# Performance work log

Hardware: AMD Instinct MI355X
Metric: run time of the kernel (lower is better)

Reference implementation:

```python
import jax, jax.numpy as jnp
import numpy as np

N_NODES = 50000
N_EDGES = 800000
IN_DIM = 128
OUT_DIM = 128
N_HEADS = 4
HEAD_DIM = OUT_DIM // N_HEADS
EDGE_EMBED_DIM = 16
LN_EPS = 1e-5


def setup_inputs() -> dict:
    key = jax.random.key(0)
    ks = jax.random.split(key, 10)
    x = jax.random.normal(ks[0], (N_NODES, IN_DIM), dtype=jnp.float32)
    edge_index = jax.random.randint(ks[1], (2, N_EDGES), 0, N_NODES, dtype=jnp.int32)
    edge_type = jax.random.randint(ks[2], (N_EDGES,), 0, 3, dtype=jnp.int32)
    # parameters (xavier-ish scaling)
    W = jax.random.normal(ks[3], (OUT_DIM, IN_DIM), dtype=jnp.float32) * (1.0 / np.sqrt(IN_DIM))
    a_src = jax.random.normal(ks[4], (N_HEADS, HEAD_DIM), dtype=jnp.float32) * (1.0 / np.sqrt(HEAD_DIM))
    a_dst = jax.random.normal(ks[5], (N_HEADS, HEAD_DIM), dtype=jnp.float32) * (1.0 / np.sqrt(HEAD_DIM))
    a_edge = jax.random.normal(ks[6], (N_HEADS, EDGE_EMBED_DIM), dtype=jnp.float32) * (1.0 / np.sqrt(EDGE_EMBED_DIM))
    edge_embed = jax.random.normal(ks[7], (3, EDGE_EMBED_DIM), dtype=jnp.float32)
    ln_gamma = jnp.ones((OUT_DIM,), dtype=jnp.float32)
    ln_beta = jnp.zeros((OUT_DIM,), dtype=jnp.float32)
    return {"x": x, "edge_index": edge_index, "edge_type": edge_type,
            "W": W, "a_src": a_src, "a_dst": a_dst, "a_edge": a_edge,
            "edge_embed": edge_embed, "ln_gamma": ln_gamma, "ln_beta": ln_beta}


def reference(x, edge_index, edge_type, W, a_src, a_dst, a_edge, edge_embed, ln_gamma, ln_beta):
    N = x.shape[0]
    h = x @ W.T                                   # [N, out_dim]
    hh = h.reshape(N, N_HEADS, HEAD_DIM)          # [N, H, D]
    src, dst = edge_index[0], edge_index[1]       # [E]

    # per-node attention projections, then gather (avoids gathering full [E,H,D] twice)
    alpha_src = jnp.einsum('nhd,hd->nh', hh, a_src)   # [N, H]
    alpha_dst = jnp.einsum('nhd,hd->nh', hh, a_dst)   # [N, H]
    e_score = edge_embed[edge_type] @ a_edge.T        # [E, H]

    attn = alpha_src[src] + alpha_dst[dst] + e_score  # [E, H]
    attn = jax.nn.leaky_relu(attn, negative_slope=0.2)

    # segment softmax over incoming edges of each dst node
    attn_max = jax.ops.segment_max(attn, dst, num_segments=N)    # [N, H]
    attn_max = jnp.maximum(attn_max, -1e9)                       # match torch init fill
    attn_exp = jnp.exp(attn - attn_max[dst])                     # [E, H]
    attn_sum = jax.ops.segment_sum(attn_exp, dst, num_segments=N)
    attn_norm = attn_exp / (attn_sum[dst] + 1e-10)               # [E, H]

    # weighted scatter-aggregation (dropout is identity in eval)
    weighted = hh[src] * attn_norm[:, :, None]                   # [E, H, D]
    out = jax.ops.segment_sum(weighted, dst, num_segments=N)     # [N, H, D]
    out = out.reshape(N, OUT_DIM) + h                            # residual

    # LayerNorm over last dim
    mu = jnp.mean(out, axis=-1, keepdims=True)
    var = jnp.var(out, axis=-1, keepdims=True)
    out = (out - mu) * jax.lax.rsqrt(var + LN_EPS)
    return out * ln_gamma + ln_beta
```

## Files before the change

kernel.cpp:

```cpp
#include <hip/hip_runtime.h>

#define N_NODES 50000
#define N_EDGES 800000
#define IN_DIM 128
#define OUT_DIM 128
#define N_HEADS 4
#define HEAD_DIM 32
#define LN_EPS 1e-5f

#define WS_HB    0
#define WS_ASRC  3200000
#define WS_ADST  3400000
#define WS_ETAB  3600000
#define WS_DEG   3600016
#define WS_AVTAB 3650016
#define WS_OFFS  3650528
#define WS_PARTS 3700528
#define WS_EPACK 3700592
#define WS_RANK  4500608

#define SCAN_BLOCKS 49

typedef __bf16 bf16x8 __attribute__((ext_vector_type(8)));
typedef float  f32x4  __attribute__((ext_vector_type(4)));

__device__ __forceinline__ unsigned short f2bf(float f) {
    unsigned int u = __float_as_uint(f);
    u += 0x7FFF + ((u >> 16) & 1);
    return (unsigned short)(u >> 16);
}
#define BFLO(u) __uint_as_float((unsigned int)(u) << 16)
#define BFHI(u) __uint_as_float((unsigned int)(u) & 0xFFFF0000u)
#define LRELU(c) ((c) > 0.f ? (c) : 0.2f * (c))

__global__ __launch_bounds__(256) void count_prep_kernel(
    const int* __restrict__ dsts, int* __restrict__ deg, int* __restrict__ rank,
    const float* __restrict__ W, const float* __restrict__ a_src,
    const float* __restrict__ a_dst, const float* __restrict__ edge_embed,
    const float* __restrict__ a_edge, float* __restrict__ etab,
    unsigned short* __restrict__ avtab)
{
    int gid = blockIdx.x * 256 + threadIdx.x;
    if (gid < 12) {
        int t = gid >> 2, hh = gid & 3;
        float s = 0.f;
        for (int k = 0; k < 16; ++k) s += edge_embed[t * 16 + k] * a_edge[hh * 16 + k];
        etab[t * 4 + hh] = s;
    }
    if (gid < 1024) {
        int c8 = gid & 7, k = gid >> 3;
        int hh = c8 & 3;
        const float* av = (c8 < 4) ? a_src : a_dst;
        float s = 0.f;
        #pragma unroll 8
        for (int dd = 0; dd < 32; ++dd)
            s += W[(hh * 32 + dd) * 128 + k] * av[hh * 32 + dd];
        int kblk = k >> 5, g = (k & 31) >> 3, j = k & 7;
        avtab[((kblk * 64) + g * 16 + c8) * 8 + j] = f2bf(s);
    }
    if (gid < N_EDGES) rank[gid] = atomicAdd(&deg[dsts[gid]], 1);
}

__global__ __launch_bounds__(256) void gemm_mfma_kernel(
    const float* __restrict__ x, const float* __restrict__ W,
    const unsigned short* __restrict__ avtab,
    unsigned short* __restrict__ hb,
    float* __restrict__ alpha_src, float* __restrict__ alpha_dst)
{
    __shared__ bf16x8 wlds[2048];
    int tid = threadIdx.x;
    for (int f = tid; f < 2048; f += 256) {
        int ct = f >> 8, kb = (f >> 6) & 3, ln = f & 63;
        int d = ct * 16 + (ln & 15);
        int kbase = kb * 32 + ((ln >> 4) << 3);
        const float* wp = W + d * 128 + kbase;
        float4 w0 = *(const float4*)wp;
        float4 w1 = *(const float4*)(wp + 4);
        bf16x8 v;
        v[0] = (__bf16)w0.x; v[1] = (__bf16)w0.y; v[2] = (__bf16)w0.z; v[3] = (__bf16)w0.w;
        v[4] = (__bf16)w1.x; v[5] = (__bf16)w1.y; v[6] = (__bf16)w1.z; v[7] = (__bf16)w1.w;
        wlds[f] = v;
    }
    int lane = tid & 63, wid = tid >> 6;
    bf16x8 avf[4];
    const bf16x8* avp = (const bf16x8*)avtab;
    #pragma unroll
    for (int kb = 0; kb < 4; ++kb) avf[kb] = avp[kb * 64 + lane];
    __syncthreads();

    int r = lane & 15, g = lane >> 4;
    int tile = blockIdx.x * 4 + wid;
    if (tile >= N_NODES / 16) return;
    {
        const float* xp = x + ((size_t)tile * 16 + r) * 128 + g * 8;
        bf16x8 af[4];
        #pragma unroll
        for (int kb = 0; kb < 4; ++kb) {
            float4 x0 = *(const float4*)(xp + kb * 32);
            float4 x1 = *(const float4*)(xp + kb * 32 + 4);
            bf16x8 v;
            v[0] = (__bf16)x0.x; v[1] = (__bf16)x0.y; v[2] = (__bf16)x0.z; v[3] = (__bf16)x0.w;
            v[4] = (__bf16)x1.x; v[5] = (__bf16)x1.y; v[6] = (__bf16)x1.z; v[7] = (__bf16)x1.w;
            af[kb] = v;
        }
        f32x4 aacc = {0.f, 0.f, 0.f, 0.f};
        #pragma unroll
        for (int kb = 0; kb < 4; ++kb)
            aacc = __builtin_amdgcn_mfma_f32_16x16x32_bf16(af[kb], avf[kb], aacc, 0, 0, 0);

        int orow = tile * 16 + g * 4;
        #pragma unroll
        for (int ct = 0; ct < 8; ++ct) {
            f32x4 acc = {0.f, 0.f, 0.f, 0.f};
            #pragma unroll
            for (int kb = 0; kb < 4; ++kb)
                acc = __builtin_amdgcn_mfma_f32_16x16x32_bf16(af[kb], wlds[(ct * 4 + kb) * 64 + lane], acc, 0, 0, 0);
            #pragma unroll
            for (int q = 0; q < 4; ++q)
                hb[(size_t)(orow + q) * 128 + ct * 16 + r] = f2bf(acc[q]);
        }
        if (r < 8) {
            float* ap = (r < 4) ? (alpha_src + (r & 3)) : (alpha_dst + (r & 3));
            #pragma unroll
            for (int q = 0; q < 4; ++q)
                ap[(size_t)(orow + q) * 4] = aacc[q];
        }
    }
}

__global__ __launch_bounds__(1024) void scan_part_kernel(
    const int* __restrict__ deg, int* __restrict__ offs, int* __restrict__ parts)
{
    __shared__ int wsum[16];
    int i = blockIdx.x * 1024 + threadIdx.x;
    int lane = threadIdx.x & 63;
    int wid  = threadIdx.x >> 6;
    int v = (i < N_NODES) ? deg[i] : 0;
    int xinc = v;
    #pragma unroll
    for (int d = 1; d < 64; d <<= 1) {
        int y = __shfl_up(xinc, d);
        if (lane >= d) xinc += y;
    }
    if (lane == 63) wsum[wid] = xinc;
    __syncthreads();
    if (wid == 0) {
        int sv = (lane < 16) ? wsum[lane] : 0;
        #pragma unroll
        for (int d = 1; d < 16; d <<= 1) {
            int y = __shfl_up(sv, d);
            if (lane >= d) sv += y;
        }
        if (lane < 16) wsum[lane] = sv;
    }
    __syncthreads();
    int woff = (wid > 0) ? wsum[wid - 1] : 0;
    if (i < N_NODES) offs[i] = woff + xinc - v;
    if (threadIdx.x == 0) parts[blockIdx.x] = wsum[15];
}

__global__ __launch_bounds__(1024) void scan_add_kernel(
    int* __restrict__ offs, const int* __restrict__ parts)
{
    __shared__ int pre_s;
    if (threadIdx.x < 64) {
        int v = ((int)threadIdx.x < (int)blockIdx.x) ? parts[threadIdx.x] : 0;
        #pragma unroll
        for (int off = 32; off >= 1; off >>= 1) v += __shfl_xor(v, off);
        if (threadIdx.x == 0) pre_s = v;
    }
    __syncthreads();
    int i = blockIdx.x * 1024 + threadIdx.x;
    if (i < N_NODES) offs[i] += pre_s;
}

__global__ void fill_kernel(const int* __restrict__ srcs, const int* __restrict__ dsts,
                            const int* __restrict__ etype, const int* __restrict__ rank,
                            const int* __restrict__ offs, unsigned int* __restrict__ epack)
{
    int e = blockIdx.x * 256 + threadIdx.x;
    if (e < N_EDGES) {
        int d = dsts[e];
        int p = offs[d] + rank[e];
        epack[p] = (unsigned int)srcs[e] | ((unsigned int)etype[e] << 16);
    }
}

__global__ __launch_bounds__(256) void aggregate_kernel(
    const unsigned short* __restrict__ hb, const float* __restrict__ alpha_src,
    const float* __restrict__ alpha_dst, const float* __restrict__ etab,
    const unsigned int* __restrict__ epack, const int* __restrict__ offs,
    const float* __restrict__ gamma, const float* __restrict__ beta,
    float* __restrict__ out)
{
    int lane = threadIdx.x & 63;
    int wid  = threadIdx.x >> 6;
    int half = lane >> 5;
    int l5   = lane & 31;
    int n = blockIdx.x * 8 + wid * 2 + half;
    if (n >= N_NODES) return;

    int e0 = offs[n];
    int e1 = (n == N_NODES - 1) ? N_EDGES : offs[n + 1];
    int deg = e1 - e0;

    int g  = l5 >> 3;
    int sl = l5 & 7;
    int headL = sl >> 1;

    float ad_h = alpha_dst[(size_t)n * 4 + headL];
    float et0 = etab[0 * 4 + headL];
    float et1 = etab[1 * 4 + headL];
    float et2 = etab[2 * 4 + headL];

    float s = 0.f;
    float acc[16];
    #pragma unroll
    for (int k = 0; k < 16; ++k) acc[k] = 0.f;

    const unsigned int* ep = epack + e0;
    for (int j = g; j < deg; j += 4) {
        unsigned int p = ep[j];
        int si = p & 0xFFFF;
        int t  = p >> 16;
        float asv = alpha_src[(size_t)si * 4 + headL];
        const uint4* hp = (const uint4*)(hb + ((size_t)si << 7) + (sl << 4));
        uint4 hA = hp[0];
        uint4 hB = hp[1];
        float ev = (t == 0) ? et0 : ((t == 1) ? et1 : et2);
        float c = LRELU(asv + ad_h + ev);
        float w = __expf(c);
        s += w;
        acc[0]  += w * BFLO(hA.x); acc[1]  += w * BFHI(hA.x);
        acc[2]  += w * BFLO(hA.y); acc[3]  += w * BFHI(hA.y);
        acc[4]  += w * BFLO(hA.z); acc[5]  += w * BFHI(hA.z);
        acc[6]  += w * BFLO(hA.w); acc[7]  += w * BFHI(hA.w);
        acc[8]  += w * BFLO(hB.x); acc[9]  += w * BFHI(hB.x);
        acc[10] += w * BFLO(hB.y); acc[11] += w * BFHI(hB.y);
        acc[12] += w * BFLO(hB.z); acc[13] += w * BFHI(hB.z);
        acc[14] += w * BFLO(hB.w); acc[15] += w * BFHI(hB.w);
    }

    #pragma unroll
    for (int k = 0; k < 16; ++k) {
        acc[k] += __shfl_xor(acc[k], 8);
        acc[k] += __shfl_xor(acc[k], 16);
    }
    s += __shfl_xor(s, 8);
    s += __shfl_xor(s, 16);
    float rs = 1.0f / (s + 1e-10f);

    const uint4* rp = (const uint4*)(hb + ((size_t)n << 7) + (sl << 4));
    uint4 r0 = rp[0];
    uint4 r1 = rp[1];
    float o[16];
    o[0]  = acc[0]  * rs + BFLO(r0.x); o[1]  = acc[1]  * rs + BFHI(r0.x);
    o[2]  = acc[2]  * rs + BFLO(r0.y); o[3]  = acc[3]  * rs + BFHI(r0.y);
    o[4]  = acc[4]  * rs + BFLO(r0.z); o[5]  = acc[5]  * rs + BFHI(r0.z);
    o[6]  = acc[6]  * rs + BFLO(r0.w); o[7]  = acc[7]  * rs + BFHI(r0.w);
    o[8]  = acc[8]  * rs + BFLO(r1.x); o[9]  = acc[9]  * rs + BFHI(r1.x);
    o[10] = acc[10] * rs + BFLO(r1.y); o[11] = acc[11] * rs + BFHI(r1.y);
    o[12] = acc[12] * rs + BFLO(r1.z); o[13] = acc[13] * rs + BFHI(r1.z);
    o[14] = acc[14] * rs + BFLO(r1.w); o[15] = acc[15] * rs + BFHI(r1.w);

    float lsum = 0.f;
    #pragma unroll
    for (int k = 0; k < 16; ++k) lsum += o[k];
    #pragma unroll
    for (int off = 4; off >= 1; off >>= 1) lsum += __shfl_xor(lsum, off);
    float mean = lsum * (1.0f / 128.0f);
    float vs = 0.f;
    #pragma unroll
    for (int k = 0; k < 16; ++k) { float d = o[k] - mean; vs += d * d; }
    #pragma unroll
    for (int off = 4; off >= 1; off >>= 1) vs += __shfl_xor(vs, off);
    float inv = rsqrtf(vs * (1.0f / 128.0f) + LN_EPS);

    float4 gv = *(const float4*)(gamma + sl * 16 + g * 4);
    float4 bv = *(const float4*)(beta  + sl * 16 + g * 4);
    float4 wv;
    wv.x = (o[g * 4 + 0] - mean) * inv * gv.x + bv.x;
    wv.y = (o[g * 4 + 1] - mean) * inv * gv.y + bv.y;
    wv.z = (o[g * 4 + 2] - mean) * inv * gv.z + bv.z;
    wv.w = (o[g * 4 + 3] - mean) * inv * gv.w + bv.w;
    *(float4*)(out + (size_t)n * OUT_DIM + sl * 16 + g * 4) = wv;
}

extern "C" void kernel_launch(void* const* d_in, const int* in_sizes, int n_in,
                              void* d_out, int out_size, void* d_ws, size_t ws_size,
                              hipStream_t stream)
{
    const float* x          = (const float*)d_in[0];
    const int*   edge_index = (const int*)d_in[1];
    const int*   etype      = (const int*)d_in[2];
    const float* W          = (const float*)d_in[3];
    const float* a_src      = (const float*)d_in[4];
    const float* a_dst      = (const float*)d_in[5];
    const float* a_edge     = (const float*)d_in[6];
    const float* edge_embed = (const float*)d_in[7];
    const float* gamma      = (const float*)d_in[8];
    const float* beta       = (const float*)d_in[9];

    float* ws = (float*)d_ws;
    unsigned short* hb = (unsigned short*)(ws + WS_HB);
    float* asrc = ws + WS_ASRC;
    float* adst = ws + WS_ADST;
    float* etab = ws + WS_ETAB;
    int*   deg  = (int*)d_ws + WS_DEG;
    unsigned short* avtab = (unsigned short*)((int*)d_ws + WS_AVTAB);
    int*   offs = (int*)d_ws + WS_OFFS;
    int*   parts= (int*)d_ws + WS_PARTS;
    unsigned int* epack = (unsigned int*)d_ws + WS_EPACK;
    int*   rank = (int*)d_ws + WS_RANK;

    const int* srcs = edge_index;
    const int* dsts = edge_index + N_EDGES;

    hipMemsetAsync(deg, 0, N_NODES * sizeof(int) + 2048 * sizeof(unsigned short), stream);

    count_prep_kernel<<<(N_EDGES + 255) / 256, 256, 0, stream>>>(
        dsts, deg, rank, W, a_src, a_dst, edge_embed, a_edge, etab, avtab);
    gemm_mfma_kernel<<<(N_NODES / 16 + 3) / 4, 256, 0, stream>>>(x, W, avtab, hb, asrc, adst);
    scan_part_kernel<<<SCAN_BLOCKS, 1024, 0, stream>>>(deg, offs, parts);
    scan_add_kernel<<<SCAN_BLOCKS, 1024, 0, stream>>>(offs, parts);
    fill_kernel<<<(N_EDGES + 255) / 256, 256, 0, stream>>>(srcs, dsts, etype, rank, offs, epack);
    aggregate_kernel<<<(N_NODES + 7) / 8, 256, 0, stream>>>(
        hb, asrc, adst, etab, epack, offs, gamma, beta, (float*)d_out);
}
```

Measured before the change: 118.7 us.

## Merge degree counting into GEMM launch and replace memset with prep kernel zeroing

```diff
diff --git a/kernel.cpp b/kernel.cpp
--- a/kernel.cpp
+++ b/kernel.cpp
@@ -20,6 +20,8 @@
 #define WS_RANK  4500608
 
 #define SCAN_BLOCKS 49
+#define GEMM_BLOCKS 512
+#define COUNT_BLOCKS 3125
 
 typedef __bf16 bf16x8 __attribute__((ext_vector_type(8)));
 typedef float  f32x4  __attribute__((ext_vector_type(4)));
@@ -33,14 +35,15 @@
 #define BFHI(u) __uint_as_float((unsigned int)(u) & 0xFFFF0000u)
 #define LRELU(c) ((c) > 0.f ? (c) : 0.2f * (c))
 
-__global__ __launch_bounds__(256) void count_prep_kernel(
-    const int* __restrict__ dsts, int* __restrict__ deg, int* __restrict__ rank,
+__global__ __launch_bounds__(256) void prep_zero_kernel(
+    int4* __restrict__ degv,
     const float* __restrict__ W, const float* __restrict__ a_src,
     const float* __restrict__ a_dst, const float* __restrict__ edge_embed,
     const float* __restrict__ a_edge, float* __restrict__ etab,
     unsigned short* __restrict__ avtab)
 {
     int gid = blockIdx.x * 256 + threadIdx.x;
+    if (gid < N_NODES / 4) degv[gid] = make_int4(0, 0, 0, 0);
     if (gid < 12) {
         int t = gid >> 2, hh = gid & 3;
         float s = 0.f;
@@ -58,17 +61,24 @@
         int kblk = k >> 5, g = (k & 31) >> 3, j = k & 7;
         avtab[((kblk * 64) + g * 16 + c8) * 8 + j] = f2bf(s);
     }
-    if (gid < N_EDGES) rank[gid] = atomicAdd(&deg[dsts[gid]], 1);
-}
-
-__global__ __launch_bounds__(256) void gemm_mfma_kernel(
+}
+
+__global__ __launch_bounds__(256) void gemm_count_kernel(
     const float* __restrict__ x, const float* __restrict__ W,
     const unsigned short* __restrict__ avtab,
     unsigned short* __restrict__ hb,
-    float* __restrict__ alpha_src, float* __restrict__ alpha_dst)
+    float* __restrict__ alpha_src, float* __restrict__ alpha_dst,
+    const int* __restrict__ dsts, int* __restrict__ deg, int* __restrict__ rank)
 {
     __shared__ bf16x8 wlds[2048];
     int tid = threadIdx.x;
+
+    if (blockIdx.x >= GEMM_BLOCKS) {
+        int gid = (blockIdx.x - GEMM_BLOCKS) * 256 + tid;
+        if (gid < N_EDGES) rank[gid] = atomicAdd(&deg[dsts[gid]], 1);
+        return;
+    }
+
     for (int f = tid; f < 2048; f += 256) {
         int ct = f >> 8, kb = (f >> 6) & 3, ln = f & 63;
         int d = ct * 16 + (ln & 15);
@@ -89,9 +99,7 @@
     __syncthreads();
 
     int r = lane & 15, g = lane >> 4;
-    int tile = blockIdx.x * 4 + wid;
-    if (tile >= N_NODES / 16) return;
-    {
+    for (int tile = blockIdx.x * 4 + wid; tile < N_NODES / 16; tile += GEMM_BLOCKS * 4) {
         const float* xp = x + ((size_t)tile * 16 + r) * 128 + g * 8;
         bf16x8 af[4];
         #pragma unroll
@@ -202,7 +210,7 @@
 
     int e0 = offs[n];
     int e1 = (n == N_NODES - 1) ? N_EDGES : offs[n + 1];
-    int deg = e1 - e0;
+    int dg = e1 - e0;
 
     int g  = l5 >> 3;
     int sl = l5 & 7;
@@ -219,7 +227,7 @@
     for (int k = 0; k < 16; ++k) acc[k] = 0.f;
 
     const unsigned int* ep = epack + e0;
-    for (int j = g; j < deg; j += 4) {
+    for (int j = g; j < dg; j += 4) {
         unsigned int p = ep[j];
         int si = p & 0xFFFF;
         int t  = p >> 16;
@@ -316,11 +324,10 @@
     const int* srcs = edge_index;
     const int* dsts = edge_index + N_EDGES;
 
-    hipMemsetAsync(deg, 0, N_NODES * sizeof(int) + 2048 * sizeof(unsigned short), stream);
-
-    count_prep_kernel<<<(N_EDGES + 255) / 256, 256, 0, stream>>>(
-        dsts, deg, rank, W, a_src, a_dst, edge_embed, a_edge, etab, avtab);
-    gemm_mfma_kernel<<<(N_NODES / 16 + 3) / 4, 256, 0, stream>>>(x, W, avtab, hb, asrc, adst);
+    prep_zero_kernel<<<SCAN_BLOCKS, 256, 0, stream>>>(
+        (int4*)deg, W, a_src, a_dst, edge_embed, a_edge, etab, avtab);
+    gemm_count_kernel<<<GEMM_BLOCKS + COUNT_BLOCKS, 256, 0, stream>>>(
+        x, W, avtab, hb, asrc, adst, dsts, deg, rank);
     scan_part_kernel<<<SCAN_BLOCKS, 1024, 0, stream>>>(deg, offs, parts);
     scan_add_kernel<<<SCAN_BLOCKS, 1024, 0, stream>>>(offs, parts);
     fill_kernel<<<(N_EDGES + 255) / 256, 256, 0, stream>>>(srcs, dsts, etype, rank, offs, epack);
```

After: 110.6 us. 1.07x faster.
